# Performance work log

Measured on AMD Instinct MI355X. Metric: run time of the kernel, lower is better.

## Reference

```python
import jax, jax.numpy as jnp
from jax import lax
import numpy as np

NODE_COUNT = 4096
BATCH = 128
THRESHOLD = 1.0
DISSIPATION = 0.1
SPARSITY = 0.9
MAX_ITERS = 100


def setup_inputs() -> dict:
    key = jax.random.key(0)
    k_in, k_conn, k_mask, k_w, k_b = jax.random.split(key, 5)
    input_data = jax.random.normal(k_in, (BATCH, NODE_COUNT), dtype=jnp.float32)
    conn = jax.random.normal(k_conn, (NODE_COUNT, NODE_COUNT), dtype=jnp.float32)
    mask = (jax.random.uniform(k_mask, (NODE_COUNT, NODE_COUNT)) > SPARSITY).astype(jnp.float32)
    conn = conn * mask
    conn = conn / (jnp.abs(conn).sum(axis=1, keepdims=True) + 1e-6)
    # input_proj: Linear(node_count, node_count), torch default init scale
    bound = 1.0 / np.sqrt(NODE_COUNT)
    W = jax.random.uniform(k_w, (NODE_COUNT, NODE_COUNT), minval=-bound, maxval=bound, dtype=jnp.float32)
    b = jax.random.uniform(k_b, (NODE_COUNT,), minval=-bound, maxval=bound, dtype=jnp.float32)
    return {"input_data": input_data, "W": W, "b": b, "connections": conn}


def _avalanche(state, connections):
    """Batched avalanche scan with per-sample sticky early-exit (torch break)."""
    B = state.shape[0]
    done0 = jnp.zeros((B,), dtype=bool)
    total0 = jnp.zeros((B,), dtype=state.dtype)

    def step(carry, _):
        state, done, total = carry
        active = (state > THRESHOLD).astype(state.dtype)          # [B, N]
        n_active = active.sum(axis=1)                              # [B]
        new_done = done | (n_active == 0)                          # break condition
        total = total + jnp.where(new_done, 0.0, n_active)
        # propagated = connections @ active  (per sample)
        prop = jnp.einsum('ij,bj->bi', connections, active)        # [B, N]
        new_state = (state * (1.0 - DISSIPATION) + prop * (1.0 - active)) * (1.0 - active)
        state = jnp.where(new_done[:, None], state, new_state)
        return (state, new_done, total), None

    (state, done, total), _ = lax.scan(step, (state, done0, total0), None, length=MAX_ITERS)
    return state, total


def reference(input_data, W, b, connections):
    projected = input_data @ W.T + b                               # [B, N]
    output, sizes = _avalanche(projected, connections)
    max_size = sizes.max()
    return output, max_size
```

## Files before the change

kernel.cpp:

```cpp
#include <hip/hip_runtime.h>

#define N_NODES 4096
#define BATCH 128
#define SPLITK 16
#define GBN 128
#define GBK 32
#define KCHUNK (N_NODES / SPLITK)
#define NSTEP (KCHUNK / GBK)
#define GEMM_BLOCKS ((N_NODES / GBN) * SPLITK)
#define TRANS_BLOCKS (32 * 32)

typedef _Float16 f16x4 __attribute__((ext_vector_type(4)));
typedef _Float16 f16x8 __attribute__((ext_vector_type(8)));
typedef float f32x4 __attribute__((ext_vector_type(4)));
typedef unsigned int u32x4 __attribute__((ext_vector_type(4)));

__device__ __forceinline__ void dma16(const void* g, void* l) {
#if defined(__has_builtin) && __has_builtin(__builtin_amdgcn_global_load_lds)
  __builtin_amdgcn_global_load_lds((const __attribute__((address_space(1))) void*)g,
                                   (__attribute__((address_space(3))) void*)l, 16, 0, 0);
#else
  *(u32x4*)l = *(const u32x4*)g;
#endif
}

#if defined(__has_builtin)
#if __has_builtin(__builtin_amdgcn_cvt_f32_fp8) && __has_builtin(__builtin_amdgcn_cvt_pk_fp8_f32)
#define CONN_FP8 1
#endif
#endif
#ifndef CONN_FP8
#define CONN_FP8 0
#endif

#if CONN_FP8
#define CONN_ELEM_BYTES 1
#define CONN_SCALE (1.0f / 256.0f)
#else
#define CONN_ELEM_BYTES 2
#define CONN_SCALE 1.0f
#endif

__device__ __forceinline__ void conn_store4(void* out, size_t off, float4 v) {
#if CONN_FP8
  unsigned int p = __builtin_amdgcn_cvt_pk_fp8_f32(v.x * 256.0f, v.y * 256.0f, 0, false);
  p = (unsigned int)__builtin_amdgcn_cvt_pk_fp8_f32(v.z * 256.0f, v.w * 256.0f, (int)p, true);
  *(unsigned int*)((unsigned char*)out + off) = p;
#else
  const unsigned int ux = __float_as_uint(v.x), uy = __float_as_uint(v.y);
  const unsigned int uz = __float_as_uint(v.z), uw = __float_as_uint(v.w);
  ushort4 u;
  u.x = (unsigned short)((ux + 0x7FFFu + ((ux >> 16) & 1u)) >> 16);
  u.y = (unsigned short)((uy + 0x7FFFu + ((uy >> 16) & 1u)) >> 16);
  u.z = (unsigned short)((uz + 0x7FFFu + ((uz >> 16) & 1u)) >> 16);
  u.w = (unsigned short)((uw + 0x7FFFu + ((uw >> 16) & 1u)) >> 16);
  *(ushort4*)((unsigned short*)out + off) = u;
#endif
}

__device__ __forceinline__ float4 conn_load4(const void* cT, int j, int t) {
#if CONN_FP8
  const unsigned int c = *(const unsigned int*)((const unsigned char*)cT + ((size_t)j << 12) + t * 4);
  return make_float4(__builtin_amdgcn_cvt_f32_fp8(c, 0), __builtin_amdgcn_cvt_f32_fp8(c, 1),
                     __builtin_amdgcn_cvt_f32_fp8(c, 2), __builtin_amdgcn_cvt_f32_fp8(c, 3));
#else
  const ushort4 c = *(const ushort4*)((const unsigned short*)cT + ((size_t)j << 12) + t * 4);
  return make_float4(__uint_as_float((unsigned int)c.x << 16),
                     __uint_as_float((unsigned int)c.y << 16),
                     __uint_as_float((unsigned int)c.z << 16),
                     __uint_as_float((unsigned int)c.w << 16));
#endif
}

__global__ __launch_bounds__(256) void asplit_kernel(const float* __restrict__ in,
                                                     _Float16* __restrict__ As,
                                                     unsigned int* __restrict__ maxslot) {
  if (blockIdx.x == 0 && threadIdx.x == 0) *maxslot = 0u;
  const size_t idx = ((size_t)blockIdx.x * 256 + threadIdx.x) * 4;
  const int m = (int)(idx >> 12);
  const int k = (int)(idx & (N_NODES - 1));
  const float4 v = *(const float4*)(in + idx);
  f16x4 hi, lo;
  const float x0 = v.x * 256.f, x1 = v.y * 256.f, x2 = v.z * 256.f, x3 = v.w * 256.f;
  hi[0] = (_Float16)x0; lo[0] = (_Float16)(x0 - (float)hi[0]);
  hi[1] = (_Float16)x1; lo[1] = (_Float16)(x1 - (float)hi[1]);
  hi[2] = (_Float16)x2; lo[2] = (_Float16)(x2 - (float)hi[2]);
  hi[3] = (_Float16)x3; lo[3] = (_Float16)(x3 - (float)hi[3]);
  const size_t base = (size_t)m * 8192 + (size_t)(k >> 5) * 64 + (k & 31);
  *(f16x4*)(As + base) = hi;
  *(f16x4*)(As + base + 32) = lo;
}

__global__ __launch_bounds__(256, 2) void transpose_kernel(const float* __restrict__ conn,
                                                           void* __restrict__ connT) {
  __shared__ float T[128][129];
  const int tid = threadIdx.x;
  const int d = blockIdx.x;
  const int by = (d & 7) | ((d >> 8) << 3);
  const int bx = (d >> 3) & 31;

  const int rr = tid >> 4;
  const int c0 = (tid & 15) * 4;
#pragma unroll
  for (int pass = 0; pass < 8; ++pass) {
    const int r = pass * 16 + rr;
    const float* src = conn + (size_t)(by * 128 + r) * N_NODES + bx * 128;
    const float4 a = *(const float4*)(src + c0);
    const float4 b = *(const float4*)(src + c0 + 64);
    *(float4*)&T[r][c0] = a;
    *(float4*)&T[r][c0 + 64] = b;
  }
  __syncthreads();

  const int jr = tid >> 5;
  const int lc = tid & 31;
#pragma unroll
  for (int pass = 0; pass < 16; ++pass) {
    const int jj = pass * 8 + jr;
    float4 v;
    v.x = T[lc * 4 + 0][jj];
    v.y = T[lc * 4 + 1][jj];
    v.z = T[lc * 4 + 2][jj];
    v.w = T[lc * 4 + 3][jj];
    conn_store4(connT, (size_t)(bx * 128 + jj) * N_NODES + by * 128 + lc * 4, v);
  }
}

struct GemmSmem {
  alignas(16) _Float16 A[2][128 * 64];
  alignas(16) float B[2][128 * 32];
};

__global__ __launch_bounds__(256, 2) void gemm_kernel(const _Float16* __restrict__ As,
                                                      const float* __restrict__ W,
                                                      float* __restrict__ P) {
  __shared__ GemmSmem sm;
  const int tid = threadIdx.x;
  const int d = blockIdx.x;
  const int ntile = (d & 7) | ((d >> 7) << 3);
  const int kidx = (d >> 3) & 15;
  const int wave = tid >> 6, lane = tid & 63;
  const int wm = wave >> 1, wn = wave & 1;
  const int g = lane >> 4, lrow = lane & 15;
  const int n0 = ntile * GBN;
  const int kb = kidx * KCHUNK;
  const int crow = lane >> 3;
  const int q = lane & 7;

  auto issue = [&](int buf, int t) {
    const size_t abyte = (size_t)((kb >> 5) + t) * 128;
    const size_t bbyte = (size_t)(kb + t * GBK) * 4;
#pragma unroll
    for (int i = 0; i < 4; ++i) {
      const int c = wave * 4 + i;
      const int row = c * 8 + crow;
      dma16((const char*)As + (size_t)row * 16384 + abyte + ((q ^ crow) << 4),
            (char*)sm.A[buf] + c * 1024 + lane * 16);
    }
#pragma unroll
    for (int i = 0; i < 4; ++i) {
      const int c = wave * 4 + i;
      const int row = c * 8 + crow;
      dma16((const char*)W + (size_t)(n0 + row) * 16384 + bbyte + ((q ^ crow) << 4),
            (char*)sm.B[buf] + c * 1024 + lane * 16);
    }
  };

  f32x4 acc[4][4] = {};
  issue(0, 0);
  issue(1, 1);

#pragma unroll
  for (int t = 0; t < NSTEP; ++t) {
    const int cur = t & 1;
    if (t + 1 < NSTEP) asm volatile("s_waitcnt vmcnt(8)" ::: "memory");
    else               asm volatile("s_waitcnt vmcnt(0)" ::: "memory");
    __builtin_amdgcn_sched_barrier(0);
    __builtin_amdgcn_s_barrier();
    __builtin_amdgcn_sched_barrier(0);

    f16x8 ah[4], al[4];
#pragma unroll
    for (int fm = 0; fm < 4; ++fm) {
      const int mr = wm * 64 + fm * 16 + lrow;
      const char* ab = (const char*)sm.A[cur] + mr * 128;
      const int s = (mr & 7) << 4;
      ah[fm] = *(const f16x8*)(ab + ((g << 4) ^ s));
      al[fm] = *(const f16x8*)(ab + (((4 + g) << 4) ^ s));
    }
    f16x8 bh[4], bl[4];
#pragma unroll
    for (int fn = 0; fn < 4; ++fn) {
      const int nr = wn * 64 + fn * 16 + lrow;
      const char* bb = (const char*)sm.B[cur] + nr * 128;
      const int s = (nr & 7) << 4;
      const f32x4 b0 = *(const f32x4*)(bb + (((2 * g) << 4) ^ s));
      const f32x4 b1 = *(const f32x4*)(bb + (((2 * g + 1) << 4) ^ s));
#pragma unroll
      for (int j = 0; j < 4; ++j) {
        const float x = b0[j] * 64.f;
        const _Float16 h = (_Float16)x;
        bh[fn][j] = h; bl[fn][j] = (_Float16)(x - (float)h);
        const float y = b1[j] * 64.f;
        const _Float16 h2 = (_Float16)y;
        bh[fn][4 + j] = h2; bl[fn][4 + j] = (_Float16)(y - (float)h2);
      }
    }
    __builtin_amdgcn_s_setprio(1);
#pragma unroll
    for (int fm = 0; fm < 4; ++fm)
#pragma unroll
      for (int fn = 0; fn < 4; ++fn) {
        acc[fm][fn] = __builtin_amdgcn_mfma_f32_16x16x32_f16(ah[fm], bh[fn], acc[fm][fn], 0, 0, 0);
        acc[fm][fn] = __builtin_amdgcn_mfma_f32_16x16x32_f16(ah[fm], bl[fn], acc[fm][fn], 0, 0, 0);
        acc[fm][fn] = __builtin_amdgcn_mfma_f32_16x16x32_f16(al[fm], bh[fn], acc[fm][fn], 0, 0, 0);
      }
    __builtin_amdgcn_s_setprio(0);

    __builtin_amdgcn_sched_barrier(0);
    __builtin_amdgcn_s_barrier();
    __builtin_amdgcn_sched_barrier(0);
    if (t + 2 < NSTEP) issue(cur, t + 2);
  }

  constexpr float INV = 1.0f / 16384.0f;
  float* Pb = P + (size_t)kidx * BATCH * N_NODES;
#pragma unroll
  for (int fm = 0; fm < 4; ++fm)
#pragma unroll
    for (int fn = 0; fn < 4; ++fn) {
      const int n = n0 + wn * 64 + fn * 16 + lrow;
#pragma unroll
      for (int reg = 0; reg < 4; ++reg) {
        const int m = wm * 64 + fm * 16 + g * 4 + reg;
        Pb[(size_t)m * N_NODES + n] = acc[fm][fn][reg] * INV;
      }
    }
}

__global__ __launch_bounds__(256) void proj_gemm_valu(const float* __restrict__ A,
                                                      const float* __restrict__ W,
                                                      float* __restrict__ P,
                                                      unsigned int* __restrict__ maxslot) {
  if (blockIdx.x == 0 && threadIdx.x == 0) *maxslot = 0u;
  __shared__ float Asb[16][132];
  __shared__ float Bsb[16][68];
  const int tid = threadIdx.x;
  const int n0 = blockIdx.x * 64;
  const int tx = tid & 15, ty = tid >> 4;
  const int arow = tid >> 1, acol = (tid & 1) * 8;
  const int brow = tid >> 2, bcol = (tid & 3) * 4;
  float acc[2][4][4] = {};
  const float* Aptr = A + (size_t)arow * N_NODES + acol;
  const float* Wptr = W + (size_t)(n0 + brow) * N_NODES + bcol;
  for (int k0 = 0; k0 < N_NODES; k0 += 16) {
    const float4 a0 = *(const float4*)(Aptr + k0);
    const float4 a1 = *(const float4*)(Aptr + k0 + 4);
    const float4 bv = *(const float4*)(Wptr + k0);
    __syncthreads();
    Asb[acol + 0][arow] = a0.x; Asb[acol + 1][arow] = a0.y;
    Asb[acol + 2][arow] = a0.z; Asb[acol + 3][arow] = a0.w;
    Asb[acol + 4][arow] = a1.x; Asb[acol + 5][arow] = a1.y;
    Asb[acol + 6][arow] = a1.z; Asb[acol + 7][arow] = a1.w;
    Bsb[bcol + 0][brow] = bv.x; Bsb[bcol + 1][brow] = bv.y;
    Bsb[bcol + 2][brow] = bv.z; Bsb[bcol + 3][brow] = bv.w;
    __syncthreads();
#pragma unroll
    for (int kk = 0; kk < 16; ++kk) {
      const float4 av0 = *(const float4*)&Asb[kk][ty * 4];
      const float4 av1 = *(const float4*)&Asb[kk][64 + ty * 4];
      const float4 bv4 = *(const float4*)&Bsb[kk][tx * 4];
      const float am[8] = {av0.x, av0.y, av0.z, av0.w, av1.x, av1.y, av1.z, av1.w};
      const float bn[4] = {bv4.x, bv4.y, bv4.z, bv4.w};
#pragma unroll
      for (int i2 = 0; i2 < 2; ++i2)
#pragma unroll
        for (int i = 0; i < 4; ++i)
#pragma unroll
          for (int j = 0; j < 4; ++j)
            acc[i2][i][j] += am[i2 * 4 + i] * bn[j];
    }
  }
#pragma unroll
  for (int i2 = 0; i2 < 2; ++i2)
#pragma unroll
    for (int i = 0; i < 4; ++i) {
      const int m = i2 * 64 + ty * 4 + i;
      *(float4*)(P + (size_t)m * N_NODES + n0 + tx * 4) =
          make_float4(acc[i2][i][0], acc[i2][i][1], acc[i2][i][2], acc[i2][i][3]);
    }
}

__global__ __launch_bounds__(256) void bias_inplace_kernel(float* __restrict__ P,
                                                           const float* __restrict__ bias) {
  const size_t base = ((size_t)blockIdx.x * 256 + threadIdx.x) * 4;
  const int n = (int)(base & (N_NODES - 1));
  float4 s = *(const float4*)(P + base);
  const float4 bv = *(const float4*)(bias + n);
  s.x += bv.x; s.y += bv.y; s.z += bv.z; s.w += bv.w;
  *(float4*)(P + base) = s;
}

template <int MODE, int NSPLIT>
__global__ __launch_bounds__(1024) void avalanche_kernel(const float* __restrict__ Pin,
                                                         const float* __restrict__ bias,
                                                         const void* __restrict__ connv,
                                                         float* __restrict__ out,
                                                         unsigned int* __restrict__ maxslot) {
  const int b = blockIdx.x;
  const int t = threadIdx.x;
  __shared__ unsigned long long mask[64];
  __shared__ int wincl[64];
  __shared__ int list[N_NODES];

  float4 s;
  if (MODE == 1) {
    const float4 bv = *(const float4*)(bias + t * 4);
    s = bv;
#pragma unroll
    for (int sp = 0; sp < NSPLIT; ++sp) {
      const float4 v = *(const float4*)(Pin + (size_t)sp * BATCH * N_NODES +
                                        (size_t)b * N_NODES + t * 4);
      s.x += v.x; s.y += v.y; s.z += v.z; s.w += v.w;
    }
  } else {
    s = *(const float4*)(Pin + (size_t)b * N_NODES + t * 4);
  }

  float total = 0.0f;

  for (int it = 0; it < 100; ++it) {
    const float v0 = s.x, v1 = s.y, v2 = s.z, v3 = s.w;
    unsigned int bits = 0;
    if (v0 > 1.0f) bits |= 1u;
    if (v1 > 1.0f) bits |= 2u;
    if (v2 > 1.0f) bits |= 4u;
    if (v3 > 1.0f) bits |= 8u;

    __syncthreads();
    if (t < 64) mask[t] = 0ULL;
    __syncthreads();
    if (bits) atomicOr(&mask[t >> 4], (unsigned long long)bits << ((t & 15) * 4));
    __syncthreads();

    if (t < 64) {
      int incl = __popcll(mask[t]);
#pragma unroll
      for (int d = 1; d < 64; d <<= 1) {
        const int y = __shfl_up(incl, d);
        if (t >= d) incl += y;
      }
      wincl[t] = incl;
    }
    __syncthreads();
    const int n = wincl[63];
    if (n == 0) break;
    total += (float)n;

    if (t < 64) {
      unsigned long long m = mask[t];
      int o = wincl[t] - __popcll(m);
      while (m) {
        list[o++] = (t << 6) + __builtin_ctzll(m);
        m &= m - 1;
      }
    }
    __syncthreads();

    float4 a0 = make_float4(0.f, 0.f, 0.f, 0.f), a1 = a0, a2 = a0, a3 = a0;
    if (MODE == 1) {
      int idx = 0;
      for (; idx + 8 <= n; idx += 8) {
        const float4 c0 = conn_load4(connv, list[idx + 0], t);
        const float4 c1 = conn_load4(connv, list[idx + 1], t);
        const float4 c2 = conn_load4(connv, list[idx + 2], t);
        const float4 c3 = conn_load4(connv, list[idx + 3], t);
        const float4 c4 = conn_load4(connv, list[idx + 4], t);
        const float4 c5 = conn_load4(connv, list[idx + 5], t);
        const float4 c6 = conn_load4(connv, list[idx + 6], t);
        const float4 c7 = conn_load4(connv, list[idx + 7], t);
        a0.x += c0.x; a0.y += c0.y; a0.z += c0.z; a0.w += c0.w;
        a1.x += c1.x; a1.y += c1.y; a1.z += c1.z; a1.w += c1.w;
        a2.x += c2.x; a2.y += c2.y; a2.z += c2.z; a2.w += c2.w;
        a3.x += c3.x; a3.y += c3.y; a3.z += c3.z; a3.w += c3.w;
        a0.x += c4.x; a0.y += c4.y; a0.z += c4.z; a0.w += c4.w;
        a1.x += c5.x; a1.y += c5.y; a1.z += c5.z; a1.w += c5.w;
        a2.x += c6.x; a2.y += c6.y; a2.z += c6.z; a2.w += c6.w;
        a3.x += c7.x; a3.y += c7.y; a3.z += c7.z; a3.w += c7.w;
      }
      for (; idx < n; ++idx) {
        const float4 c = conn_load4(connv, list[idx], t);
        a0.x += c.x; a0.y += c.y; a0.z += c.z; a0.w += c.w;
      }
    } else {
      const float* conn = (const float*)connv;
      for (int idx = 0; idx < n; ++idx) {
        const int j = list[idx];
        a0.x += conn[(size_t)(t * 4 + 0) * N_NODES + j];
        a0.y += conn[(size_t)(t * 4 + 1) * N_NODES + j];
        a0.z += conn[(size_t)(t * 4 + 2) * N_NODES + j];
        a0.w += conn[(size_t)(t * 4 + 3) * N_NODES + j];
      }
    }
    const float sc = (MODE == 1) ? CONN_SCALE : 1.0f;
    const float4 acc = make_float4(((a0.x + a1.x) + (a2.x + a3.x)) * sc,
                                   ((a0.y + a1.y) + (a2.y + a3.y)) * sc,
                                   ((a0.z + a1.z) + (a2.z + a3.z)) * sc,
                                   ((a0.w + a1.w) + (a2.w + a3.w)) * sc);

    s.x = (v0 > 1.0f) ? 0.0f : 0.9f * v0 + acc.x;
    s.y = (v1 > 1.0f) ? 0.0f : 0.9f * v1 + acc.y;
    s.z = (v2 > 1.0f) ? 0.0f : 0.9f * v2 + acc.z;
    s.w = (v3 > 1.0f) ? 0.0f : 0.9f * v3 + acc.w;
  }

  *(float4*)(out + (size_t)b * N_NODES + t * 4) = s;
  if (t == 0) atomicMax(maxslot, __float_as_uint(total));
}

extern "C" void kernel_launch(void* const* d_in, const int* in_sizes, int n_in,
                              void* d_out, int out_size, void* d_ws, size_t ws_size,
                              hipStream_t stream) {
  const float* input = (const float*)d_in[0];
  const float* W     = (const float*)d_in[1];
  const float* bias  = (const float*)d_in[2];
  const float* conn  = (const float*)d_in[3];
  float* out = (float*)d_out;

  const size_t aplane_bytes = (size_t)BATCH * N_NODES * 4;
  const size_t connT_bytes  = (size_t)N_NODES * N_NODES * CONN_ELEM_BYTES;
  const size_t part_bytes   = (size_t)SPLITK * BATCH * N_NODES * sizeof(float);
  unsigned int* maxslot = (unsigned int*)(out + (size_t)BATCH * N_NODES);

  if (ws_size >= aplane_bytes + connT_bytes + part_bytes) {
    _Float16* As = (_Float16*)d_ws;
    void* connT  = (char*)d_ws + aplane_bytes;
    float* part  = (float*)((char*)d_ws + aplane_bytes + connT_bytes);
    asplit_kernel<<<BATCH * N_NODES / 1024, 256, 0, stream>>>(input, As, maxslot);
    transpose_kernel<<<TRANS_BLOCKS, 256, 0, stream>>>(conn, connT);
    gemm_kernel<<<GEMM_BLOCKS, 256, 0, stream>>>(As, W, part);
    avalanche_kernel<1, SPLITK><<<BATCH, 1024, 0, stream>>>(part, bias, connT, out, maxslot);
  } else {
    proj_gemm_valu<<<dim3(N_NODES / 64, 1), 256, 0, stream>>>(input, W, out, maxslot);
    bias_inplace_kernel<<<BATCH * N_NODES / 1024, 256, 0, stream>>>(out, bias);
    avalanche_kernel<0, 1><<<BATCH, 1024, 0, stream>>>(out, nullptr, conn, out, maxslot);
  }
}
```

Baseline: 71.34 us.

## Halve GEMM N-tile, drop double buffering, raise occupancy to four blocks

The split-K GEMM kernel's N tile shrinks from 128 to 64, which doubles the number of blocks. Shared memory becomes a single buffer, so the two-stage prefetch pipeline is replaced by a load, __syncthreads, compute, __syncthreads loop. Launch bounds now ask for 4 blocks per CU, and the block index mapping is simplified to put kidx in the low bits. The aim is to hide latency through occupancy rather than software pipelining. The trade-off is that load/compute overlap within a block is lost, each B fragment is reused across fewer MFMAs, and A is loaded redundantly twice as often.

```diff
diff --git a/kernel.cpp b/kernel.cpp
--- a/kernel.cpp
+++ b/kernel.cpp
@@ -3,7 +3,7 @@
 #define N_NODES 4096
 #define BATCH 128
 #define SPLITK 16
-#define GBN 128
+#define GBN 64
 #define GBK 32
 #define KCHUNK (N_NODES / SPLITK)
 #define NSTEP (KCHUNK / GBK)
@@ -127,18 +127,18 @@
 }
 
 struct GemmSmem {
-  alignas(16) _Float16 A[2][128 * 64];
-  alignas(16) float B[2][128 * 32];
+  alignas(16) _Float16 A[128 * 64];
+  alignas(16) float B[GBN * 32];
 };
 
-__global__ __launch_bounds__(256, 2) void gemm_kernel(const _Float16* __restrict__ As,
+__global__ __launch_bounds__(256, 4) void gemm_kernel(const _Float16* __restrict__ As,
                                                       const float* __restrict__ W,
                                                       float* __restrict__ P) {
   __shared__ GemmSmem sm;
   const int tid = threadIdx.x;
-  const int d = blockIdx.x;
-  const int ntile = (d & 7) | ((d >> 7) << 3);
-  const int kidx = (d >> 3) & 15;
+  const int bid = blockIdx.x;
+  const int kidx = bid & 15;
+  const int ntile = bid >> 4;
   const int wave = tid >> 6, lane = tid & 63;
   const int wm = wave >> 1, wn = wave & 1;
   const int g = lane >> 4, lrow = lane & 15;
@@ -147,7 +147,7 @@
   const int crow = lane >> 3;
   const int q = lane & 7;
 
-  auto issue = [&](int buf, int t) {
+  auto issue = [&](int t) {
     const size_t abyte = (size_t)((kb >> 5) + t) * 128;
     const size_t bbyte = (size_t)(kb + t * GBK) * 4;
 #pragma unroll
@@ -155,44 +155,38 @@
       const int c = wave * 4 + i;
       const int row = c * 8 + crow;
       dma16((const char*)As + (size_t)row * 16384 + abyte + ((q ^ crow) << 4),
-            (char*)sm.A[buf] + c * 1024 + lane * 16);
-    }
-#pragma unroll
-    for (int i = 0; i < 4; ++i) {
-      const int c = wave * 4 + i;
+            (char*)sm.A + c * 1024 + lane * 16);
+    }
+#pragma unroll
+    for (int i = 0; i < 2; ++i) {
+      const int c = wave * 2 + i;
       const int row = c * 8 + crow;
       dma16((const char*)W + (size_t)(n0 + row) * 16384 + bbyte + ((q ^ crow) << 4),
-            (char*)sm.B[buf] + c * 1024 + lane * 16);
+            (char*)sm.B + c * 1024 + lane * 16);
     }
   };
 
-  f32x4 acc[4][4] = {};
-  issue(0, 0);
-  issue(1, 1);
+  f32x4 acc[4][2] = {};
 
 #pragma unroll
   for (int t = 0; t < NSTEP; ++t) {
-    const int cur = t & 1;
-    if (t + 1 < NSTEP) asm volatile("s_waitcnt vmcnt(8)" ::: "memory");
-    else               asm volatile("s_waitcnt vmcnt(0)" ::: "memory");
-    __builtin_amdgcn_sched_barrier(0);
-    __builtin_amdgcn_s_barrier();
-    __builtin_amdgcn_sched_barrier(0);
+    issue(t);
+    __syncthreads();
 
     f16x8 ah[4], al[4];
 #pragma unroll
     for (int fm = 0; fm < 4; ++fm) {
       const int mr = wm * 64 + fm * 16 + lrow;
-      const char* ab = (const char*)sm.A[cur] + mr * 128;
+      const char* ab = (const char*)sm.A + mr * 128;
       const int s = (mr & 7) << 4;
       ah[fm] = *(const f16x8*)(ab + ((g << 4) ^ s));
       al[fm] = *(const f16x8*)(ab + (((4 + g) << 4) ^ s));
     }
-    f16x8 bh[4], bl[4];
-#pragma unroll
-    for (int fn = 0; fn < 4; ++fn) {
-      const int nr = wn * 64 + fn * 16 + lrow;
-      const char* bb = (const char*)sm.B[cur] + nr * 128;
+    f16x8 bh[2], bl[2];
+#pragma unroll
+    for (int fn = 0; fn < 2; ++fn) {
+      const int nr = wn * 32 + fn * 16 + lrow;
+      const char* bb = (const char*)sm.B + nr * 128;
       const int s = (nr & 7) << 4;
       const f32x4 b0 = *(const f32x4*)(bb + (((2 * g) << 4) ^ s));
       const f32x4 b1 = *(const f32x4*)(bb + (((2 * g + 1) << 4) ^ s));
@@ -206,21 +200,15 @@
         bh[fn][4 + j] = h2; bl[fn][4 + j] = (_Float16)(y - (float)h2);
       }
     }
-    __builtin_amdgcn_s_setprio(1);
 #pragma unroll
     for (int fm = 0; fm < 4; ++fm)
 #pragma unroll
-      for (int fn = 0; fn < 4; ++fn) {
+      for (int fn = 0; fn < 2; ++fn) {
         acc[fm][fn] = __builtin_amdgcn_mfma_f32_16x16x32_f16(ah[fm], bh[fn], acc[fm][fn], 0, 0, 0);
         acc[fm][fn] = __builtin_amdgcn_mfma_f32_16x16x32_f16(ah[fm], bl[fn], acc[fm][fn], 0, 0, 0);
         acc[fm][fn] = __builtin_amdgcn_mfma_f32_16x16x32_f16(al[fm], bh[fn], acc[fm][fn], 0, 0, 0);
       }
-    __builtin_amdgcn_s_setprio(0);
-
-    __builtin_amdgcn_sched_barrier(0);
-    __builtin_amdgcn_s_barrier();
-    __builtin_amdgcn_sched_barrier(0);
-    if (t + 2 < NSTEP) issue(cur, t + 2);
+    __syncthreads();
   }
 
   constexpr float INV = 1.0f / 16384.0f;
@@ -228,8 +216,8 @@
 #pragma unroll
   for (int fm = 0; fm < 4; ++fm)
 #pragma unroll
-    for (int fn = 0; fn < 4; ++fn) {
-      const int n = n0 + wn * 64 + fn * 16 + lrow;
+    for (int fn = 0; fn < 2; ++fn) {
+      const int n = n0 + wn * 32 + fn * 16 + lrow;
 #pragma unroll
       for (int reg = 0; reg < 4; ++reg) {
         const int m = wm * 64 + fm * 16 + g * 4 + reg;
```

Result: no change. 71.19 us (-0.2%).
